# Kernel tuning notes

Hardware: AMD Instinct MI355X
Metric: run time of the kernel (lower is better)

Reference implementation:

```python
import jax, jax.numpy as jnp
import numpy as np

N_NODES = 50000
N_EDGES = 800000
F_IN = 128
HID = 32
HEADS = 8
NEG_SLOPE = 0.2  # PyG GATConv default leaky_relu slope


def gat_conv(x, src, dst, W, a_src, a_dst, b, num_nodes):
    """PyG-style GATConv (eval mode, self-loops already included in src/dst).
    W: [F_in, H*C], a_src/a_dst: [H, C], b: [H*C]."""
    H, C = a_src.shape
    h = (x @ W).reshape(num_nodes, H, C)                      # [N,H,C]
    alpha_s = jnp.einsum('nhc,hc->nh', h, a_src)              # [N,H]
    alpha_d = jnp.einsum('nhc,hc->nh', h, a_dst)
    e = jax.nn.leaky_relu(alpha_s[src] + alpha_d[dst], NEG_SLOPE)  # [E,H]
    # numerically-stable softmax over edges grouped by destination node
    m = jax.ops.segment_max(e, dst, num_segments=num_nodes)  # [N,H]
    e = jnp.exp(e - m[dst])
    denom = jax.ops.segment_sum(e, dst, num_segments=num_nodes)
    alpha = e / denom[dst]                                    # [E,H]
    msg = h[src] * alpha[:, :, None]                          # [E,H,C]
    out = jax.ops.segment_sum(msg, dst, num_segments=num_nodes)  # [N,H,C]
    return out.reshape(num_nodes, H * C) + b


def setup_inputs() -> dict:
    key = jax.random.key(0)
    ks = jax.random.split(key, 10)
    x = jax.random.normal(ks[0], (N_NODES, F_IN), dtype=jnp.float32)
    edge_index = jax.random.randint(ks[1], (2, N_EDGES), 0, N_NODES, dtype=jnp.int64)
    s = 0.1
    W1 = jax.random.normal(ks[2], (F_IN, HEADS * HID), dtype=jnp.float32) * s
    att_src1 = jax.random.normal(ks[3], (HEADS, HID), dtype=jnp.float32) * s
    att_dst1 = jax.random.normal(ks[4], (HEADS, HID), dtype=jnp.float32) * s
    b1 = jnp.zeros((HEADS * HID,), dtype=jnp.float32)
    W2 = jax.random.normal(ks[5], (HEADS * HID, HID), dtype=jnp.float32) * s
    att_src2 = jax.random.normal(ks[6], (1, HID), dtype=jnp.float32) * s
    att_dst2 = jax.random.normal(ks[7], (1, HID), dtype=jnp.float32) * s
    b2 = jnp.zeros((HID,), dtype=jnp.float32)
    return {"x": x, "edge_index": edge_index, "W1": W1, "att_src1": att_src1,
            "att_dst1": att_dst1, "b1": b1, "W2": W2, "att_src2": att_src2,
            "att_dst2": att_dst2, "b2": b2}


def reference(x, edge_index, W1, att_src1, att_dst1, b1, W2, att_src2, att_dst2, b2):
    num_nodes = x.shape[0]
    # PyG GATConv adds self-loops by default
    loop = jnp.arange(num_nodes, dtype=edge_index.dtype)
    src = jnp.concatenate([edge_index[0], loop])
    dst = jnp.concatenate([edge_index[1], loop])
    h = gat_conv(x, src, dst, W1, att_src1, att_dst1, b1, num_nodes)  # [N, 8*HID]
    h = jax.nn.elu(h)
    # dropout is identity in eval mode
    out = gat_conv(h, src, dst, W2, att_src2, att_dst2, b2, num_nodes)  # [N, HID]
    return out
```

## Files before the change

kernel.cpp:

```cpp
#include <hip/hip_runtime.h>

#define F_IN 128
#define HC1 256
#define HID 32
#define HEADS 8
#define MAXDEG 64

#define BW    256
#define NB    196
#define NR    8
#define RCAP  768
#define BCAP  64
#define CHUNK 4096

typedef _Float16 h16;
typedef h16 f16x2 __attribute__((ext_vector_type(2)));
typedef h16 f16x4 __attribute__((ext_vector_type(4)));
typedef h16 f16x8 __attribute__((ext_vector_type(8)));
typedef float f32x4 __attribute__((ext_vector_type(4)));

union U2 { unsigned u; f16x2 h; };
union U4 { uint2 u; f16x4 h4; f16x2 h2[2]; };
union U8 { uint4 u; f16x8 h8; f16x2 h2[4]; };

__device__ __forceinline__ unsigned pkexp(float t){
  t = fminf(fmaxf(t, -30.f), 5.f);
  U2 r; r.h = (f16x2){ (h16)__expf(t), (h16)__expf(0.2f*t) };
  return r.u;
}

__global__ void k_prep(const float* __restrict__ w1, const float* __restrict__ w2,
                       const float* __restrict__ as1w, const float* __restrict__ ad1w,
                       h16* __restrict__ w1t, h16* __restrict__ w2t,
                       h16* __restrict__ awt, int* __restrict__ gcur){
  int t = blockIdx.x*blockDim.x + threadIdx.x;
  if (t < NB*NR) gcur[t] = 0;
  if (t < HC1*F_IN){
    int n = t >> 7, k = t & 127;
    w1t[t] = (h16)w1[(size_t)k*HC1 + n];
  } else if (t < HC1*F_IN + HID*HC1){
    int u = t - HC1*F_IN;
    int n = u >> 8, k = u & 255;
    w2t[u] = (h16)w2[(size_t)k*HID + n];
  } else if (t < HC1*F_IN + HID*HC1 + 16*F_IN){
    int u = t - HC1*F_IN - HID*HC1;
    int c = u >> 7, k = u & 127;
    int h = c & 7;
    const float* a = (c < 8) ? as1w : ad1w;
    float s = 0.f;
    #pragma unroll
    for (int j = 0; j < 32; ++j) s += w1[(size_t)k*HC1 + h*HID + j] * a[h*HID + j];
    awt[u] = (h16)s;
  }
}

__global__ __launch_bounds__(256) void k_bin(const int* __restrict__ srcA,
    const int* __restrict__ dstA, int* __restrict__ gcur,
    uint2* __restrict__ rec, int E){
  __shared__ int   cl[NB];
  __shared__ int   bl[NB];
  __shared__ uint2 buf[NB][BCAP];
  int tid = threadIdx.x;
  for (int t = tid; t < NB; t += 256) cl[t] = 0;
  __syncthreads();
  int e0 = blockIdx.x*CHUNK;
  #pragma unroll
  for (int j = 0; j < CHUNK; j += 256){
    int e = e0 + j + tid;
    if (e < E){
      int d = dstA[e], s = srcA[e];
      int b = d >> 8;
      int p = atomicAdd(&cl[b], 1);
      if (p < BCAP) buf[b][p] = make_uint2((unsigned)d, (unsigned)s);
    }
  }
  __syncthreads();
  int r = blockIdx.x & (NR-1);
  if (tid < NB){
    int c = cl[tid]; if (c > BCAP) c = BCAP;
    cl[tid] = c;
    bl[tid] = (c > 0) ? atomicAdd(&gcur[tid*NR + r], c) : 0;
  }
  __syncthreads();
  int wv = tid >> 6, lane = tid & 63;
  for (int b = wv; b < NB; b += 4){
    int c = cl[b];
    if (lane < c){
      int idx = bl[b] + lane;
      if (idx < RCAP) rec[(size_t)(b*NR + r)*RCAP + idx] = buf[b][lane];
    }
  }
}

__global__ __launch_bounds__(256) void k_csr(const uint2* __restrict__ rec,
    const int* __restrict__ gcur, int* __restrict__ cnt, int* __restrict__ csr, int N){
  __shared__ int cl[BW];
  int tid = threadIdx.x;
  int b = blockIdx.x;
  if (tid < BW) cl[tid] = 0;
  __syncthreads();
  for (int r = 0; r < NR; ++r){
    int len = gcur[b*NR + r]; if (len > RCAP) len = RCAP;
    const uint2* rr = rec + (size_t)(b*NR + r)*RCAP;
    for (int i = tid; i < len; i += 256){
      uint2 v = rr[i];
      int d = (int)v.x, s = (int)v.y;
      int slot = atomicAdd(&cl[d & (BW-1)], 1);
      if (slot < MAXDEG) csr[d*MAXDEG + slot] = s;
    }
  }
  __syncthreads();
  int d = b*BW + tid;
  if (tid < BW && d < N) cnt[d] = cl[tid];
}

__global__ __launch_bounds__(256) void k_gemm1(const float* __restrict__ x,
    const h16* __restrict__ w1t, const h16* __restrict__ awt,
    h16* __restrict__ h1h,
    unsigned* __restrict__ es1p, unsigned* __restrict__ ed1p, int M){
  int tid = threadIdx.x;
  __shared__ h16 As[64][136];
  __shared__ h16 Bs[64][136];
  __shared__ h16 Aw[16][136];
  int rowbase = blockIdx.x * 64;
  #pragma unroll
  for (int j = 0; j < 8; ++j){
    int idx = (tid + 256*j) * 4;
    int r = idx >> 7, c = idx & 127;
    int row = rowbase + r;
    float4 v = make_float4(0.f,0.f,0.f,0.f);
    if (row < M) v = *(const float4*)(x + (size_t)row*F_IN + c);
    U4 q; q.h4 = (f16x4){ (h16)v.x, (h16)v.y, (h16)v.z, (h16)v.w };
    *(uint2*)&As[r][c] = q.u;
  }
  {
    int idx = tid * 8;
    int c = idx >> 7, k = idx & 127;
    *(uint4*)&Aw[c][k] = *(const uint4*)(awt + idx);
  }
  int wv = tid >> 6, lane = tid & 63;
  int lr = lane & 15, lq = lane >> 4;
  int mrow = wv*16 + lr;

  #pragma unroll
  for (int q = 0; q < 4; ++q){
    __syncthreads();
    #pragma unroll
    for (int j = 0; j < 4; ++j){
      int idx = (tid + 256*j) * 8;
      int r = idx >> 7, c = idx & 127;
      *(uint4*)&Bs[r][c] = *(const uint4*)(w1t + (size_t)(q*64 + r)*F_IN + c);
    }
    __syncthreads();
    f32x4 acc[4] = {};
    #pragma unroll
    for (int k0 = 0; k0 < F_IN; k0 += 32){
      f16x8 a = *(const f16x8*)&As[mrow][k0 + lq*8];
      #pragma unroll
      for (int cb = 0; cb < 4; ++cb){
        f16x8 b = *(const f16x8*)&Bs[cb*16 + lr][k0 + lq*8];
        acc[cb] = __builtin_amdgcn_mfma_f32_16x16x32_f16(a, b, acc[cb], 0, 0, 0);
      }
    }
    #pragma unroll
    for (int cb = 0; cb < 4; ++cb){
      #pragma unroll
      for (int r = 0; r < 4; ++r){
        int row = rowbase + wv*16 + lq*4 + r;
        int col = q*64 + cb*16 + lr;
        if (row < M) h1h[(size_t)row*HC1 + col] = (h16)acc[cb][r];
      }
    }
  }
  {
    f32x4 aacc = {};
    #pragma unroll
    for (int k0 = 0; k0 < F_IN; k0 += 32){
      f16x8 a = *(const f16x8*)&As[mrow][k0 + lq*8];
      f16x8 b = *(const f16x8*)&Aw[lr][k0 + lq*8];
      aacc = __builtin_amdgcn_mfma_f32_16x16x32_f16(a, b, aacc, 0, 0, 0);
    }
    int h = lr & 7;
    unsigned* dstp = (lr < 8) ? es1p : ed1p;
    #pragma unroll
    for (int r = 0; r < 4; ++r){
      int row = rowbase + wv*16 + lq*4 + r;
      if (row < M) dstp[row*HEADS + h] = pkexp(aacc[r]);
    }
  }
}

__global__ __launch_bounds__(256) void k_agg1(const h16* __restrict__ h1h,
    const unsigned* __restrict__ es1p, const unsigned* __restrict__ ed1p,
    const int* __restrict__ cnt, const int* __restrict__ csr,
    const float* __restrict__ b1,
    const h16* __restrict__ w2t, const float* __restrict__ as2w,
    const float* __restrict__ ad2w,
    h16* __restrict__ g2h, unsigned* __restrict__ es2p, unsigned* __restrict__ ed2p,
    int N){
  __shared__ h16 Ws2[32][264];
  __shared__ h16 h2s[4][256];
  int tid = threadIdx.x;
  #pragma unroll
  for (int j = 0; j < 4; ++j){
    int idx = (tid + 256*j) * 8;
    int n = idx >> 8, k = idx & 255;
    *(uint4*)&Ws2[n][k] = *(const uint4*)(w2t + idx);
  }
  int wv = tid >> 6, lane = tid & 63;
  int w0 = blockIdx.x*4 + wv;
  bool valid = w0 < N;
  int w = valid ? w0 : N-1;
  int c0 = lane << 2;
  int h = lane >> 3;
  U2 ed; ed.u = ed1p[w*HEADS + h];
  U2 es; es.u = es1p[w*HEADS + h];
  f16x2 pp = es.h * ed.h;
  h16 pm = pp[0] > pp[1] ? pp[0] : pp[1];
  f16x2 pv = { pm, pm };
  U4 sv; sv.u = *(const uint2*)(h1h + (size_t)w*HC1 + c0);
  f16x2 a01 = pv * sv.h2[0];
  f16x2 a23 = pv * sv.h2[1];
  float l = (float)pm;
  int deg = cnt[w]; if (deg > MAXDEG) deg = MAXDEG;
  const int* crow = csr + w*MAXDEG;
  for (int base = 0; base < deg; base += 8){
    int s0a, s1a, s2a, s3a, s4a, s5a, s6a, s7a;
    {
      int i0=base+0,i1=base+1,i2=base+2,i3=base+3,i4=base+4,i5=base+5,i6=base+6,i7=base+7;
      int c0i=i0<MAXDEG?i0:MAXDEG-1, c1i=i1<MAXDEG?i1:MAXDEG-1;
      int c2i=i2<MAXDEG?i2:MAXDEG-1, c3i=i3<MAXDEG?i3:MAXDEG-1;
      int c4i=i4<MAXDEG?i4:MAXDEG-1, c5i=i5<MAXDEG?i5:MAXDEG-1;
      int c6i=i6<MAXDEG?i6:MAXDEG-1, c7i=i7<MAXDEG?i7:MAXDEG-1;
      int v0=crow[c0i], v1=crow[c1i], v2=crow[c2i], v3=crow[c3i];
      int v4=crow[c4i], v5=crow[c5i], v6=crow[c6i], v7=crow[c7i];
      s0a = i0<deg?v0:w; s1a = i1<deg?v1:w; s2a = i2<deg?v2:w; s3a = i3<deg?v3:w;
      s4a = i4<deg?v4:w; s5a = i5<deg?v5:w; s6a = i6<deg?v6:w; s7a = i7<deg?v7:w;
    }
    U2 e0,e1,e2,e3,e4,e5,e6,e7;
    e0.u = es1p[s0a*HEADS + h]; e1.u = es1p[s1a*HEADS + h];
    e2.u = es1p[s2a*HEADS + h]; e3.u = es1p[s3a*HEADS + h];
    e4.u = es1p[s4a*HEADS + h]; e5.u = es1p[s5a*HEADS + h];
    e6.u = es1p[s6a*HEADS + h]; e7.u = es1p[s7a*HEADS + h];
    U4 u0,u1,u2,u3,u4,u5,u6,u7;
    u0.u = *(const uint2*)(h1h + (size_t)s0a*HC1 + c0);
    u1.u = *(const uint2*)(h1h + (size_t)s1a*HC1 + c0);
    u2.u = *(const uint2*)(h1h + (size_t)s2a*HC1 + c0);
    u3.u = *(const uint2*)(h1h + (size_t)s3a*HC1 + c0);
    u4.u = *(const uint2*)(h1h + (size_t)s4a*HC1 + c0);
    u5.u = *(const uint2*)(h1h + (size_t)s5a*HC1 + c0);
    u6.u = *(const uint2*)(h1h + (size_t)s6a*HC1 + c0);
    u7.u = *(const uint2*)(h1h + (size_t)s7a*HC1 + c0);
    #define ACC1(EE,UU,II)                                      \
    { f16x2 p2 = EE.h * ed.h;                                   \
      h16 p = p2[0] > p2[1] ? p2[0] : p2[1];                    \
      p = ((base+(II)) < deg) ? p : (h16)0.f;                   \
      f16x2 pw = { p, p };                                      \
      a01 += pw * UU.h2[0]; a23 += pw * UU.h2[1];               \
      l += (float)p; }
    ACC1(e0,u0,0) ACC1(e1,u1,1) ACC1(e2,u2,2) ACC1(e3,u3,3)
    ACC1(e4,u4,4) ACC1(e5,u5,5) ACC1(e6,u6,6) ACC1(e7,u7,7)
    #undef ACC1
  }
  float rl = 1.f / l;
  float4 bb = *(const float4*)(b1 + c0);
  float o0 = (float)a01[0]*rl + bb.x;
  float o1 = (float)a01[1]*rl + bb.y;
  float o2 = (float)a23[0]*rl + bb.z;
  float o3 = (float)a23[1]*rl + bb.w;
  o0 = o0 > 0.f ? o0 : __expf(o0) - 1.f;
  o1 = o1 > 0.f ? o1 : __expf(o1) - 1.f;
  o2 = o2 > 0.f ? o2 : __expf(o2) - 1.f;
  o3 = o3 > 0.f ? o3 : __expf(o3) - 1.f;
  U4 pk; pk.h4 = (f16x4){ (h16)o0, (h16)o1, (h16)o2, (h16)o3 };
  *(uint2*)&h2s[wv][c0] = pk.u;
  __syncthreads();

  int j = lane & 31, hs = lane >> 5;
  const h16* hrow = &h2s[wv][hs*128];
  const h16* wrow = &Ws2[j][hs*128];
  f16x2 acA = {0,0}, acB = {0,0};
  #pragma unroll
  for (int cb = 0; cb < 16; ++cb){
    U8 hv, wv8;
    hv.h8  = *(const f16x8*)(hrow + cb*8);
    wv8.h8 = *(const f16x8*)(wrow + cb*8);
    acA += hv.h2[0]*wv8.h2[0];
    acB += hv.h2[1]*wv8.h2[1];
    acA += hv.h2[2]*wv8.h2[2];
    acB += hv.h2[3]*wv8.h2[3];
  }
  f16x2 ac = acA + acB;
  float g = (float)ac[0] + (float)ac[1];
  g += __shfl_xor(g, 32, 64);
  if (valid && hs == 0) g2h[(size_t)w0*HID + j] = (h16)g;
  float ps = g * as2w[j];
  float pd = g * ad2w[j];
  #pragma unroll
  for (int mask = 1; mask <= 16; mask <<= 1){
    ps += __shfl_xor(ps, mask, 64);
    pd += __shfl_xor(pd, mask, 64);
  }
  if (valid && lane == 0){
    es2p[w0] = pkexp(ps);
    ed2p[w0] = pkexp(pd);
  }
}

__global__ __launch_bounds__(256) void k_agg2(const h16* __restrict__ g2h,
    const unsigned* __restrict__ es2p, const unsigned* __restrict__ ed2p,
    const int* __restrict__ cnt, const int* __restrict__ csr,
    const float* __restrict__ b2, float* __restrict__ out, int N){
  int tid = threadIdx.x;
  int w = blockIdx.x*8 + (tid >> 6)*2 + ((tid & 63) >> 5);
  if (w >= N) return;
  int l32 = tid & 31;
  int grp = l32 >> 3;
  int cl  = l32 & 7;
  int c0 = cl << 2;
  U2 ed; ed.u = ed2p[w];
  U4 acc; acc.h2[0] = (f16x2){0,0}; acc.h2[1] = (f16x2){0,0};
  float l = 0.f;
  if (grp == 0){
    U2 es; es.u = es2p[w];
    f16x2 pp = es.h * ed.h;
    h16 pm = pp[0] > pp[1] ? pp[0] : pp[1];
    f16x2 pv = { pm, pm };
    U4 u; u.u = *(const uint2*)(g2h + (size_t)w*HID + c0);
    acc.h2[0] = pv * u.h2[0]; acc.h2[1] = pv * u.h2[1];
    l = (float)pm;
  }
  int s0 = w*MAXDEG;
  int d = cnt[w]; if (d > MAXDEG) d = MAXDEG;
  int e1 = s0 + d;
  for (int i = s0 + grp; i < e1; i += 4){
    int s = csr[i];
    U2 es; es.u = es2p[s];
    U4 u; u.u = *(const uint2*)(g2h + (size_t)s*HID + c0);
    f16x2 pp = es.h * ed.h;
    h16 pm = pp[0] > pp[1] ? pp[0] : pp[1];
    f16x2 pv = { pm, pm };
    acc.h2[0] += pv * u.h2[0];
    acc.h2[1] += pv * u.h2[1];
    l += (float)pm;
  }
  #pragma unroll
  for (int mask = 8; mask <= 16; mask <<= 1){
    l += __shfl_xor(l, mask, 64);
    U4 o;
    o.u.x = __shfl_xor(acc.u.x, mask, 64);
    o.u.y = __shfl_xor(acc.u.y, mask, 64);
    acc.h2[0] += o.h2[0]; acc.h2[1] += o.h2[1];
  }
  if (grp == 0){
    float rl = 1.f / l;
    float4 bb = *(const float4*)(b2 + c0);
    *(float4*)(out + (size_t)w*HID + c0) = make_float4(
      (float)acc.h4[0]*rl + bb.x, (float)acc.h4[1]*rl + bb.y,
      (float)acc.h4[2]*rl + bb.z, (float)acc.h4[3]*rl + bb.w);
  }
}

extern "C" void kernel_launch(void* const* d_in, const int* in_sizes, int n_in,
                              void* d_out, int out_size, void* d_ws, size_t ws_size,
                              hipStream_t stream){
  const float* x    = (const float*)d_in[0];
  const int*   ei   = (const int*)d_in[1];
  const float* W1   = (const float*)d_in[2];
  const float* as1w = (const float*)d_in[3];
  const float* ad1w = (const float*)d_in[4];
  const float* b1   = (const float*)d_in[5];
  const float* W2   = (const float*)d_in[6];
  const float* as2w = (const float*)d_in[7];
  const float* ad2w = (const float*)d_in[8];
  const float* b2   = (const float*)d_in[9];
  float* out = (float*)d_out;

  const int N = in_sizes[0] / F_IN;
  const int E = in_sizes[1] / 2;
  const int* srcA = ei;
  const int* dstA = ei + E;

  unsigned* es1p = (unsigned*)d_ws;
  unsigned* ed1p = es1p + (size_t)N*HEADS;
  unsigned* es2p = ed1p + (size_t)N*HEADS;
  unsigned* ed2p = es2p + N;
  h16* w1t = (h16*)(ed2p + N);
  h16* w2t = w1t + (size_t)HC1*F_IN;
  h16* awt = w2t + (size_t)HID*HC1;
  h16* h1h = awt + (size_t)16*F_IN;
  h16* g2h = h1h + (size_t)N*HC1;
  int* cnt = (int*)(g2h + (size_t)N*HID);
  int* csr = cnt + N;

  uint2* rec = (uint2*)h1h;
  int* gcur  = (int*)g2h;

  int prepT = HC1*F_IN + HID*HC1 + 16*F_IN;
  int prepG = (N > prepT ? N : prepT);
  k_prep <<<(prepG+255)/256, 256, 0, stream>>>(W1, W2, as1w, ad1w, w1t, w2t, awt, gcur);

  int gb = (E + CHUNK - 1)/CHUNK;
  k_bin  <<<gb, 256, 0, stream>>>(srcA, dstA, gcur, rec, E);
  k_csr  <<<NB, 256, 0, stream>>>(rec, gcur, cnt, csr, N);

  int g1 = (N + 63)/64;
  k_gemm1 <<<g1, 256, 0, stream>>>(x, w1t, awt, h1h, es1p, ed1p, N);
  k_agg1  <<<(N + 3)/4, 256, 0, stream>>>(h1h, es1p, ed1p, cnt, csr, b1,
                                          w2t, as2w, ad2w, g2h, es2p, ed2p, N);
  k_agg2  <<<(N + 7)/8, 256, 0, stream>>>(g2h, es2p, ed2p, cnt, csr, b2, out, N);
}
```

Before: 223.4 us.

## Fuse edge binning into the first GEMM kernel with a shared-memory union

```diff
diff --git a/kernel.cpp b/kernel.cpp
--- a/kernel.cpp
+++ b/kernel.cpp
@@ -10,8 +10,7 @@
 #define NB    196
 #define NR    8
 #define RCAP  768
-#define BCAP  64
-#define CHUNK 4096
+#define BCAP2 24
 
 typedef _Float16 h16;
 typedef h16 f16x2 __attribute__((ext_vector_type(2)));
@@ -54,44 +53,6 @@
   }
 }
 
-__global__ __launch_bounds__(256) void k_bin(const int* __restrict__ srcA,
-    const int* __restrict__ dstA, int* __restrict__ gcur,
-    uint2* __restrict__ rec, int E){
-  __shared__ int   cl[NB];
-  __shared__ int   bl[NB];
-  __shared__ uint2 buf[NB][BCAP];
-  int tid = threadIdx.x;
-  for (int t = tid; t < NB; t += 256) cl[t] = 0;
-  __syncthreads();
-  int e0 = blockIdx.x*CHUNK;
-  #pragma unroll
-  for (int j = 0; j < CHUNK; j += 256){
-    int e = e0 + j + tid;
-    if (e < E){
-      int d = dstA[e], s = srcA[e];
-      int b = d >> 8;
-      int p = atomicAdd(&cl[b], 1);
-      if (p < BCAP) buf[b][p] = make_uint2((unsigned)d, (unsigned)s);
-    }
-  }
-  __syncthreads();
-  int r = blockIdx.x & (NR-1);
-  if (tid < NB){
-    int c = cl[tid]; if (c > BCAP) c = BCAP;
-    cl[tid] = c;
-    bl[tid] = (c > 0) ? atomicAdd(&gcur[tid*NR + r], c) : 0;
-  }
-  __syncthreads();
-  int wv = tid >> 6, lane = tid & 63;
-  for (int b = wv; b < NB; b += 4){
-    int c = cl[b];
-    if (lane < c){
-      int idx = bl[b] + lane;
-      if (idx < RCAP) rec[(size_t)(b*NR + r)*RCAP + idx] = buf[b][lane];
-    }
-  }
-}
-
 __global__ __launch_bounds__(256) void k_csr(const uint2* __restrict__ rec,
     const int* __restrict__ gcur, int* __restrict__ cnt, int* __restrict__ csr, int N){
   __shared__ int cl[BW];
@@ -116,12 +77,49 @@
 
 __global__ __launch_bounds__(256) void k_gemm1(const float* __restrict__ x,
     const h16* __restrict__ w1t, const h16* __restrict__ awt,
+    const int* __restrict__ srcA, const int* __restrict__ dstA,
+    int* __restrict__ gcur, uint2* __restrict__ rec,
     h16* __restrict__ h1h,
-    unsigned* __restrict__ es1p, unsigned* __restrict__ ed1p, int M){
+    unsigned* __restrict__ es1p, unsigned* __restrict__ ed1p, int M, int E){
+  __shared__ union SMem {
+    struct { h16 As[64][136]; h16 Bs[64][136]; h16 Aw[16][136]; } g;
+    struct { int cl[NB]; int bl[NB]; uint2 buf[NB][BCAP2]; } b;
+  } sm;
   int tid = threadIdx.x;
-  __shared__ h16 As[64][136];
-  __shared__ h16 Bs[64][136];
-  __shared__ h16 Aw[16][136];
+
+  {
+    for (int t = tid; t < NB; t += 256) sm.b.cl[t] = 0;
+    __syncthreads();
+    int e0 = blockIdx.x * 1024;
+    #pragma unroll
+    for (int j = 0; j < 1024; j += 256){
+      int e = e0 + j + tid;
+      if (e < E){
+        int d = dstA[e], s = srcA[e];
+        int b = d >> 8;
+        int p = atomicAdd(&sm.b.cl[b], 1);
+        if (p < BCAP2) sm.b.buf[b][p] = make_uint2((unsigned)d, (unsigned)s);
+      }
+    }
+    __syncthreads();
+    int r = blockIdx.x & (NR-1);
+    if (tid < NB){
+      int c = sm.b.cl[tid]; if (c > BCAP2) c = BCAP2;
+      sm.b.cl[tid] = c;
+      sm.b.bl[tid] = (c > 0) ? atomicAdd(&gcur[tid*NR + r], c) : 0;
+    }
+    __syncthreads();
+    int wv0 = tid >> 6, lane0 = tid & 63;
+    for (int b = wv0; b < NB; b += 4){
+      int c = sm.b.cl[b];
+      if (lane0 < c){
+        int idx = sm.b.bl[b] + lane0;
+        if (idx < RCAP) rec[(size_t)(b*NR + r)*RCAP + idx] = sm.b.buf[b][lane0];
+      }
+    }
+    __syncthreads();
+  }
+
   int rowbase = blockIdx.x * 64;
   #pragma unroll
   for (int j = 0; j < 8; ++j){
@@ -131,12 +129,12 @@
     float4 v = make_float4(0.f,0.f,0.f,0.f);
     if (row < M) v = *(const float4*)(x + (size_t)row*F_IN + c);
     U4 q; q.h4 = (f16x4){ (h16)v.x, (h16)v.y, (h16)v.z, (h16)v.w };
-    *(uint2*)&As[r][c] = q.u;
+    *(uint2*)&sm.g.As[r][c] = q.u;
   }
   {
     int idx = tid * 8;
     int c = idx >> 7, k = idx & 127;
-    *(uint4*)&Aw[c][k] = *(const uint4*)(awt + idx);
+    *(uint4*)&sm.g.Aw[c][k] = *(const uint4*)(awt + idx);
   }
   int wv = tid >> 6, lane = tid & 63;
   int lr = lane & 15, lq = lane >> 4;
@@ -149,16 +147,16 @@
     for (int j = 0; j < 4; ++j){
       int idx = (tid + 256*j) * 8;
       int r = idx >> 7, c = idx & 127;
-      *(uint4*)&Bs[r][c] = *(const uint4*)(w1t + (size_t)(q*64 + r)*F_IN + c);
+      *(uint4*)&sm.g.Bs[r][c] = *(const uint4*)(w1t + (size_t)(q*64 + r)*F_IN + c);
     }
     __syncthreads();
     f32x4 acc[4] = {};
     #pragma unroll
     for (int k0 = 0; k0 < F_IN; k0 += 32){
-      f16x8 a = *(const f16x8*)&As[mrow][k0 + lq*8];
+      f16x8 a = *(const f16x8*)&sm.g.As[mrow][k0 + lq*8];
       #pragma unroll
       for (int cb = 0; cb < 4; ++cb){
-        f16x8 b = *(const f16x8*)&Bs[cb*16 + lr][k0 + lq*8];
+        f16x8 b = *(const f16x8*)&sm.g.Bs[cb*16 + lr][k0 + lq*8];
         acc[cb] = __builtin_amdgcn_mfma_f32_16x16x32_f16(a, b, acc[cb], 0, 0, 0);
       }
     }
@@ -176,8 +174,8 @@
     f32x4 aacc = {};
     #pragma unroll
     for (int k0 = 0; k0 < F_IN; k0 += 32){
-      f16x8 a = *(const f16x8*)&As[mrow][k0 + lq*8];
-      f16x8 b = *(const f16x8*)&Aw[lr][k0 + lq*8];
+      f16x8 a = *(const f16x8*)&sm.g.As[mrow][k0 + lq*8];
+      f16x8 b = *(const f16x8*)&sm.g.Aw[lr][k0 + lq*8];
       aacc = __builtin_amdgcn_mfma_f32_16x16x32_f16(a, b, aacc, 0, 0, 0);
     }
     int h = lr & 7;
@@ -392,21 +390,20 @@
   h16* g2h = h1h + (size_t)N*HC1;
   int* cnt = (int*)(g2h + (size_t)N*HID);
   int* csr = cnt + N;
-
-  uint2* rec = (uint2*)h1h;
-  int* gcur  = (int*)g2h;
+  int* gcur = csr + (size_t)N*MAXDEG;
+  uint2* rec = (uint2*)(gcur + NB*NR);
 
   int prepT = HC1*F_IN + HID*HC1 + 16*F_IN;
   int prepG = (N > prepT ? N : prepT);
   k_prep <<<(prepG+255)/256, 256, 0, stream>>>(W1, W2, as1w, ad1w, w1t, w2t, awt, gcur);
 
-  int gb = (E + CHUNK - 1)/CHUNK;
-  k_bin  <<<gb, 256, 0, stream>>>(srcA, dstA, gcur, rec, E);
+  int gN = (N + 63)/64;
+  int gE = (E + 1023)/1024;
+  int g1 = gN > gE ? gN : gE;
+  k_gemm1 <<<g1, 256, 0, stream>>>(x, w1t, awt, srcA, dstA, gcur, rec,
+                                   h1h, es1p, ed1p, N, E);
   k_csr  <<<NB, 256, 0, stream>>>(rec, gcur, cnt, csr, N);
-
-  int g1 = (N + 63)/64;
-  k_gemm1 <<<g1, 256, 0, stream>>>(x, w1t, awt, h1h, es1p, ed1p, N);
-  k_agg1  <<<(N + 3)/4, 256, 0, stream>>>(h1h, es1p, ed1p, cnt, csr, b1,
-                                          w2t, as2w, ad2w, g2h, es2p, ed2p, N);
-  k_agg2  <<<(N + 7)/8, 256, 0, stream>>>(g2h, es2p, ed2p, cnt, csr, b2, out, N);
-}
+  k_agg1 <<<(N + 3)/4, 256, 0, stream>>>(h1h, es1p, ed1p, cnt, csr, b1,
+                                         w2t, as2w, ad2w, g2h, es2p, ed2p, N);
+  k_agg2 <<<(N + 7)/8, 256, 0, stream>>>(g2h, es2p, ed2p, cnt, csr, b2, out, N);
+}
```

New measurement: 227.5 us. Within noise of the previous version (+1.8%).

## Remap agg1 lanes to one edge per lane group with dummy padded node

Applied to the files above, without the earlier changes.

```diff
diff --git a/kernel.cpp b/kernel.cpp
--- a/kernel.cpp
+++ b/kernel.cpp
@@ -32,9 +32,12 @@
 __global__ void k_prep(const float* __restrict__ w1, const float* __restrict__ w2,
                        const float* __restrict__ as1w, const float* __restrict__ ad1w,
                        h16* __restrict__ w1t, h16* __restrict__ w2t,
-                       h16* __restrict__ awt, int* __restrict__ gcur){
+                       h16* __restrict__ awt, int* __restrict__ gcur,
+                       unsigned* __restrict__ es1p, h16* __restrict__ h1h, int N){
   int t = blockIdx.x*blockDim.x + threadIdx.x;
   if (t < NB*NR) gcur[t] = 0;
+  if (t < HEADS) es1p[(size_t)N*HEADS + t] = 0;
+  if (t < HC1/2) ((unsigned*)(h1h + (size_t)N*HC1))[t] = 0;
   if (t < HC1*F_IN){
     int n = t >> 7, k = t & 127;
     w1t[t] = (h16)w1[(size_t)k*HC1 + n];
@@ -111,7 +114,13 @@
   }
   __syncthreads();
   int d = b*BW + tid;
-  if (tid < BW && d < N) cnt[d] = cl[tid];
+  if (tid < BW && d < N){
+    int c = cl[tid];
+    cnt[d] = c;
+    int cc = c > MAXDEG ? MAXDEG : c;
+    int p8 = (cc + 7) & ~7; if (p8 > MAXDEG) p8 = MAXDEG;
+    for (int j = cc; j < p8; ++j) csr[d*MAXDEG + j] = N;
+  }
 }
 
 __global__ __launch_bounds__(256) void k_gemm1(const float* __restrict__ x,
@@ -211,79 +220,87 @@
   int w0 = blockIdx.x*4 + wv;
   bool valid = w0 < N;
   int w = valid ? w0 : N-1;
-  int c0 = lane << 2;
-  int h = lane >> 3;
-  U2 ed; ed.u = ed1p[w*HEADS + h];
-  U2 es; es.u = es1p[w*HEADS + h];
-  f16x2 pp = es.h * ed.h;
-  h16 pm = pp[0] > pp[1] ? pp[0] : pp[1];
-  f16x2 pv = { pm, pm };
-  U4 sv; sv.u = *(const uint2*)(h1h + (size_t)w*HC1 + c0);
-  f16x2 a01 = pv * sv.h2[0];
-  f16x2 a23 = pv * sv.h2[1];
-  float l = (float)pm;
+  int g  = lane >> 3;
+  int c8 = lane & 7;
+  U2 ed; ed.u = ed1p[w*HEADS + c8];
   int deg = cnt[w]; if (deg > MAXDEG) deg = MAXDEG;
+  int degp = (deg + 7) & ~7;
   const int* crow = csr + w*MAXDEG;
-  for (int base = 0; base < deg; base += 8){
-    int s0a, s1a, s2a, s3a, s4a, s5a, s6a, s7a;
-    {
-      int i0=base+0,i1=base+1,i2=base+2,i3=base+3,i4=base+4,i5=base+5,i6=base+6,i7=base+7;
-      int c0i=i0<MAXDEG?i0:MAXDEG-1, c1i=i1<MAXDEG?i1:MAXDEG-1;
-      int c2i=i2<MAXDEG?i2:MAXDEG-1, c3i=i3<MAXDEG?i3:MAXDEG-1;
-      int c4i=i4<MAXDEG?i4:MAXDEG-1, c5i=i5<MAXDEG?i5:MAXDEG-1;
-      int c6i=i6<MAXDEG?i6:MAXDEG-1, c7i=i7<MAXDEG?i7:MAXDEG-1;
-      int v0=crow[c0i], v1=crow[c1i], v2=crow[c2i], v3=crow[c3i];
-      int v4=crow[c4i], v5=crow[c5i], v6=crow[c6i], v7=crow[c7i];
-      s0a = i0<deg?v0:w; s1a = i1<deg?v1:w; s2a = i2<deg?v2:w; s3a = i3<deg?v3:w;
-      s4a = i4<deg?v4:w; s5a = i5<deg?v5:w; s6a = i6<deg?v6:w; s7a = i7<deg?v7:w;
-    }
-    U2 e0,e1,e2,e3,e4,e5,e6,e7;
-    e0.u = es1p[s0a*HEADS + h]; e1.u = es1p[s1a*HEADS + h];
-    e2.u = es1p[s2a*HEADS + h]; e3.u = es1p[s3a*HEADS + h];
-    e4.u = es1p[s4a*HEADS + h]; e5.u = es1p[s5a*HEADS + h];
-    e6.u = es1p[s6a*HEADS + h]; e7.u = es1p[s7a*HEADS + h];
-    U4 u0,u1,u2,u3,u4,u5,u6,u7;
-    u0.u = *(const uint2*)(h1h + (size_t)s0a*HC1 + c0);
-    u1.u = *(const uint2*)(h1h + (size_t)s1a*HC1 + c0);
-    u2.u = *(const uint2*)(h1h + (size_t)s2a*HC1 + c0);
-    u3.u = *(const uint2*)(h1h + (size_t)s3a*HC1 + c0);
-    u4.u = *(const uint2*)(h1h + (size_t)s4a*HC1 + c0);
-    u5.u = *(const uint2*)(h1h + (size_t)s5a*HC1 + c0);
-    u6.u = *(const uint2*)(h1h + (size_t)s6a*HC1 + c0);
-    u7.u = *(const uint2*)(h1h + (size_t)s7a*HC1 + c0);
-    #define ACC1(EE,UU,II)                                      \
-    { f16x2 p2 = EE.h * ed.h;                                   \
-      h16 p = p2[0] > p2[1] ? p2[0] : p2[1];                    \
-      p = ((base+(II)) < deg) ? p : (h16)0.f;                   \
-      f16x2 pw = { p, p };                                      \
-      a01 += pw * UU.h2[0]; a23 += pw * UU.h2[1];               \
-      l += (float)p; }
-    ACC1(e0,u0,0) ACC1(e1,u1,1) ACC1(e2,u2,2) ACC1(e3,u3,3)
-    ACC1(e4,u4,4) ACC1(e5,u5,5) ACC1(e6,u6,6) ACC1(e7,u7,7)
-    #undef ACC1
-  }
-  float rl = 1.f / l;
-  float4 bb = *(const float4*)(b1 + c0);
-  float o0 = (float)a01[0]*rl + bb.x;
-  float o1 = (float)a01[1]*rl + bb.y;
-  float o2 = (float)a23[0]*rl + bb.z;
-  float o3 = (float)a23[1]*rl + bb.w;
+  int lbase = lane & 56;
+
+  f16x2 accA[8], accB[8];
+  #pragma unroll
+  for (int s_ = 0; s_ < 8; ++s_){ accA[s_] = (f16x2){0,0}; accB[s_] = (f16x2){0,0}; }
+  float lsum = 0.f;
+
+  for (int base = 0; base < degp; base += 8){
+    int s = crow[base + g];
+    U2 e; e.u = es1p[(size_t)s*HEADS + c8];
+    f16x2 pp = e.h * ed.h;
+    h16 p = pp[0] > pp[1] ? pp[0] : pp[1];
+    U2 pk_; pk_.h = (f16x2){ p, p };
+    lsum += (float)p;
+    const h16* hrow = h1h + (size_t)s*HC1 + c8*4;
+    #pragma unroll
+    for (int seg = 0; seg < 8; ++seg){
+      U2 pw; pw.u = (unsigned)__shfl((int)pk_.u, lbase | seg, 64);
+      U4 u; u.u = *(const uint2*)(hrow + seg*32);
+      accA[seg] += pw.h * u.h2[0];
+      accB[seg] += pw.h * u.h2[1];
+    }
+  }
+  #pragma unroll
+  for (int mask = 8; mask <= 32; mask <<= 1){
+    lsum += __shfl_xor(lsum, mask, 64);
+    #pragma unroll
+    for (int s_ = 0; s_ < 8; ++s_){
+      U2 a_; a_.h = accA[s_];
+      U2 b_; b_.h = accB[s_];
+      U2 a2; a2.u = (unsigned)__shfl_xor((int)a_.u, mask, 64);
+      U2 b2; b2.u = (unsigned)__shfl_xor((int)b_.u, mask, 64);
+      accA[s_] += a2.h; accB[s_] += b2.h;
+    }
+  }
+  f16x2 myA = accA[0], myB = accB[0];
+  #pragma unroll
+  for (int s_ = 1; s_ < 8; ++s_){
+    if (g == s_){ myA = accA[s_]; myB = accB[s_]; }
+  }
+  float L = __shfl(lsum, 9*g, 64);
+  {
+    U2 eS;  eS.u  = es1p[w*HEADS + g];
+    U2 edS; edS.u = ed1p[w*HEADS + g];
+    f16x2 ppS = eS.h * edS.h;
+    h16 pS = ppS[0] > ppS[1] ? ppS[0] : ppS[1];
+    f16x2 pvS = { pS, pS };
+    U4 sv; sv.u = *(const uint2*)(h1h + (size_t)w*HC1 + g*32 + c8*4);
+    myA += pvS * sv.h2[0];
+    myB += pvS * sv.h2[1];
+    L += (float)pS;
+  }
+  int col0 = g*32 + c8*4;
+  float rl = 1.f / L;
+  float4 bb = *(const float4*)(b1 + col0);
+  float o0 = (float)myA[0]*rl + bb.x;
+  float o1 = (float)myA[1]*rl + bb.y;
+  float o2 = (float)myB[0]*rl + bb.z;
+  float o3 = (float)myB[1]*rl + bb.w;
   o0 = o0 > 0.f ? o0 : __expf(o0) - 1.f;
   o1 = o1 > 0.f ? o1 : __expf(o1) - 1.f;
   o2 = o2 > 0.f ? o2 : __expf(o2) - 1.f;
   o3 = o3 > 0.f ? o3 : __expf(o3) - 1.f;
   U4 pk; pk.h4 = (f16x4){ (h16)o0, (h16)o1, (h16)o2, (h16)o3 };
-  *(uint2*)&h2s[wv][c0] = pk.u;
+  *(uint2*)&h2s[wv][col0] = pk.u;
   __syncthreads();
 
   int j = lane & 31, hs = lane >> 5;
-  const h16* hrow = &h2s[wv][hs*128];
+  const h16* hrow2 = &h2s[wv][hs*128];
   const h16* wrow = &Ws2[j][hs*128];
   f16x2 acA = {0,0}, acB = {0,0};
   #pragma unroll
   for (int cb = 0; cb < 16; ++cb){
     U8 hv, wv8;
-    hv.h8  = *(const f16x8*)(hrow + cb*8);
+    hv.h8  = *(const f16x8*)(hrow2 + cb*8);
     wv8.h8 = *(const f16x8*)(wrow + cb*8);
     acA += hv.h2[0]*wv8.h2[0];
     acB += hv.h2[1]*wv8.h2[1];
@@ -291,11 +308,11 @@
     acB += hv.h2[3]*wv8.h2[3];
   }
   f16x2 ac = acA + acB;
-  float g = (float)ac[0] + (float)ac[1];
-  g += __shfl_xor(g, 32, 64);
-  if (valid && hs == 0) g2h[(size_t)w0*HID + j] = (h16)g;
-  float ps = g * as2w[j];
-  float pd = g * ad2w[j];
+  float gg = (float)ac[0] + (float)ac[1];
+  gg += __shfl_xor(gg, 32, 64);
+  if (valid && hs == 0) g2h[(size_t)w0*HID + j] = (h16)gg;
+  float ps = gg * as2w[j];
+  float pd = gg * ad2w[j];
   #pragma unroll
   for (int mask = 1; mask <= 16; mask <<= 1){
     ps += __shfl_xor(ps, mask, 64);
@@ -335,6 +352,7 @@
   int e1 = s0 + d;
   for (int i = s0 + grp; i < e1; i += 4){
     int s = csr[i];
+    if (s >= N) continue;
     U2 es; es.u = es2p[s];
     U4 u; u.u = *(const uint2*)(g2h + (size_t)s*HID + c0);
     f16x2 pp = es.h * ed.h;
@@ -382,23 +400,23 @@
   const int* dstA = ei + E;
 
   unsigned* es1p = (unsigned*)d_ws;
-  unsigned* ed1p = es1p + (size_t)N*HEADS;
+  unsigned* ed1p = es1p + (size_t)(N+1)*HEADS;
   unsigned* es2p = ed1p + (size_t)N*HEADS;
   unsigned* ed2p = es2p + N;
   h16* w1t = (h16*)(ed2p + N);
   h16* w2t = w1t + (size_t)HC1*F_IN;
   h16* awt = w2t + (size_t)HID*HC1;
   h16* h1h = awt + (size_t)16*F_IN;
-  h16* g2h = h1h + (size_t)N*HC1;
+  h16* g2h = h1h + (size_t)(N+1)*HC1;
   int* cnt = (int*)(g2h + (size_t)N*HID);
   int* csr = cnt + N;
-
-  uint2* rec = (uint2*)h1h;
-  int* gcur  = (int*)g2h;
+  int* gcur = csr + (size_t)N*MAXDEG;
+  uint2* rec = (uint2*)(gcur + NB*NR + 2);
 
   int prepT = HC1*F_IN + HID*HC1 + 16*F_IN;
   int prepG = (N > prepT ? N : prepT);
-  k_prep <<<(prepG+255)/256, 256, 0, stream>>>(W1, W2, as1w, ad1w, w1t, w2t, awt, gcur);
+  k_prep <<<(prepG+255)/256, 256, 0, stream>>>(W1, W2, as1w, ad1w, w1t, w2t, awt,
+                                               gcur, es1p, h1h, N);
 
   int gb = (E + CHUNK - 1)/CHUNK;
   k_bin  <<<gb, 256, 0, stream>>>(srcA, dstA, gcur, rec, E);
```

Measured after the change: 236.6 us. 1.06x slower.
